# Kernel tuning notes

Measured on AMD Instinct MI355X. Metric: run time of the kernel, lower is better.

The kernel has to match this reference:

```python
import jax, jax.numpy as jnp
import numpy as np

B, L, E, H, FF = 2, 2048, 1024, 16, 4096
DH = E // H
EPS = 1e-5
# NOTE: source has attn_scale = 1 / dh**(-0.5) == sqrt(dh) (multiplies, not divides)
ATTN_SCALE = float(DH) ** 0.5


def _layernorm(x, w, b):
    mu = jnp.mean(x, axis=-1, keepdims=True)
    var = jnp.mean((x - mu) ** 2, axis=-1, keepdims=True)
    return (x - mu) * jax.lax.rsqrt(var + EPS) * w + b


def setup_inputs() -> dict:
    key = jax.random.key(0)
    ks = jax.random.split(key, 8)
    s = 0.02
    return {
        "x": jax.random.normal(ks[0], (B, L, E), jnp.float32),
        "ln1_w": jnp.ones((E,), jnp.float32),
        "ln1_b": jnp.zeros((E,), jnp.float32),
        "wq": jax.random.normal(ks[1], (E, E), jnp.float32) * s,
        "bq": jnp.zeros((E,), jnp.float32),
        "wk": jax.random.normal(ks[2], (E, E), jnp.float32) * s,
        "bk": jnp.zeros((E,), jnp.float32),
        "wv": jax.random.normal(ks[3], (E, E), jnp.float32) * s,
        "bv": jnp.zeros((E,), jnp.float32),
        "wo": jax.random.normal(ks[4], (E, E), jnp.float32) * s,
        "bo": jnp.zeros((E,), jnp.float32),
        "ln2_w": jnp.ones((E,), jnp.float32),
        "ln2_b": jnp.zeros((E,), jnp.float32),
        "wu": jax.random.normal(ks[5], (E, FF), jnp.float32) * s,
        "bu": jnp.zeros((FF,), jnp.float32),
        "wd": jax.random.normal(ks[6], (FF, E), jnp.float32) * s,
        "bd": jnp.zeros((E,), jnp.float32),
    }


def reference(x, ln1_w, ln1_b, wq, bq, wk, bk, wv, bv, wo, bo,
              ln2_w, ln2_b, wu, bu, wd, bd):
    # --- attention block (pre-LN, manual softmax attention) ---
    xn = _layernorm(x, ln1_w, ln1_b)                       # [B,L,E]
    q = (xn @ wq + bq).reshape(B, L, H, DH)
    k = (xn @ wk + bk).reshape(B, L, H, DH)
    v = (xn @ wv + bv).reshape(B, L, H, DH)
    score = jnp.einsum("blhd,bmhd->bhlm", q, k) * ATTN_SCALE  # [B,H,L,L]
    attn = jax.nn.softmax(score, axis=-1)
    ctx = jnp.einsum("bhlm,bmhd->blhd", attn, v).reshape(B, L, E)
    hidden = x + (ctx @ wo + bo)
    # --- FFN block (pre-LN, GELU) ---
    hn = _layernorm(hidden, ln2_w, ln2_b)
    up = jax.nn.gelu(hn @ wu + bu, approximate=False)      # [B,L,F]
    down = up @ wd + bd
    return hidden + down
```

## Files before the change

### kernel.cpp

```cpp
#include <hip/hip_runtime.h>
#include <stdint.h>


typedef __attribute__((ext_vector_type(8))) short short8;
typedef __attribute__((ext_vector_type(4))) float floatx4;
typedef __attribute__((ext_vector_type(16))) float floatx16;

extern "C" __device__ float __ocml_native_exp2_f32(float);
#define EXP2(x) __ocml_native_exp2_f32(x)

#define MFMA_BF16(a, b, c) __builtin_amdgcn_mfma_f32_16x16x32_bf16((a), (b), (c), 0, 0, 0)
#define MFMA32(a, b, c) __builtin_amdgcn_mfma_f32_32x32x16_bf16((a), (b), (c), 0, 0, 0)

__device__ __forceinline__ unsigned short f2bf(float f) {
  union { float f; unsigned int u; } v; v.f = f;
  unsigned int r = v.u + 0x7FFFu + ((v.u >> 16) & 1u);
  return (unsigned short)(r >> 16);
}

__device__ __forceinline__ unsigned int f2u(float f) {
  union { float f; unsigned int u; } v; v.f = f; return v.u;
}

__device__ __forceinline__ short8 pack4(unsigned a, unsigned b, unsigned c, unsigned d) {
  union { unsigned u[4]; short8 s; } v;
  v.u[0] = a; v.u[1] = b; v.u[2] = c; v.u[3] = d;
  return v.s;
}

__device__ __forceinline__ void gl_lds16(const unsigned short* g, unsigned short* l) {
  __builtin_amdgcn_global_load_lds(
      (const __attribute__((address_space(1))) unsigned int*)g,
      (__attribute__((address_space(3))) unsigned int*)l, 16, 0, 0);
}

template <int MODE, int BN>
__global__ __launch_bounds__(256)
void gemm_bt(const unsigned short* __restrict__ A,
             const unsigned short* __restrict__ Bt,
             const float* __restrict__ bias,
             void* __restrict__ outp,
             const float* __restrict__ res,
             int K,
             void* __restrict__ out2, void* __restrict__ out3,
             const float* __restrict__ bias2, const float* __restrict__ bias3) {
  constexpr int BM = 128, BK = 64;
  constexpr int MI = (BN == 128) ? 4 : 2;
  constexpr int NI = 4;
  __shared__ __align__(16) unsigned short As[BM * BK];
  __shared__ __align__(16) unsigned short Bs[BN * BK];
  const int tid = threadIdx.x;
  const int wave = tid >> 6, lane = tid & 63, l16 = lane & 15, quad = lane >> 4;
  const int m0 = blockIdx.y * BM, n0 = blockIdx.x * BN;
  const int wm = (BN == 128) ? (wave >> 1) * 64 : wave * 32;
  const int wn = (BN == 128) ? (wave & 1) * 64 : 0;
  const int sw = l16 & 7;
  const int sl0 = (quad ^ sw) << 3;
  const int sl1 = sl0 ^ 32;

  floatx4 acc[MI][NI] = {};

  for (int k0 = 0; k0 < K; k0 += BK) {
    __syncthreads();
#pragma unroll
    for (int c = 0; c < (BM * BK) / 2048; ++c) {
      const int e = (c * 256 + tid) * 8;
      const int row = e >> 6, c8 = (e >> 3) & 7;
      gl_lds16(A + (size_t)(m0 + row) * K + k0 + ((c8 ^ (row & 7)) << 3), &As[e]);
    }
#pragma unroll
    for (int c = 0; c < (BN * BK) / 2048; ++c) {
      const int e = (c * 256 + tid) * 8;
      const int row = e >> 6, c8 = (e >> 3) & 7;
      gl_lds16(Bt + (size_t)(n0 + row) * K + k0 + ((c8 ^ (row & 7)) << 3), &Bs[e]);
    }
    __syncthreads();

    short8 af0[MI], af1[MI], bf0[NI], bf1[NI];
#pragma unroll
    for (int i = 0; i < MI; ++i) {
      af0[i] = *(const short8*)&As[(wm + i * 16 + l16) * BK + sl0];
      af1[i] = *(const short8*)&As[(wm + i * 16 + l16) * BK + sl1];
    }
#pragma unroll
    for (int i = 0; i < NI; ++i) {
      bf0[i] = *(const short8*)&Bs[(wn + i * 16 + l16) * BK + sl0];
      bf1[i] = *(const short8*)&Bs[(wn + i * 16 + l16) * BK + sl1];
    }
#pragma unroll
    for (int mi = 0; mi < MI; ++mi)
#pragma unroll
      for (int ni = 0; ni < NI; ++ni) {
        acc[mi][ni] = MFMA_BF16(af0[mi], bf0[ni], acc[mi][ni]);
        acc[mi][ni] = MFMA_BF16(af1[mi], bf1[ni], acc[mi][ni]);
      }
  }

  const int seg = (MODE == 0) ? (n0 >> 10) : 0;
  const float* bptr = bias;
  if constexpr (MODE == 0) bptr = (seg == 0) ? bias : (seg == 1 ? bias2 : bias3);

  float bcol[NI];
#pragma unroll
  for (int ni = 0; ni < NI; ++ni) {
    const int n = n0 + wn + ni * 16 + l16;
    bcol[ni] = bptr[(MODE == 0) ? (n & 1023) : n];
  }

#pragma unroll
  for (int mi = 0; mi < MI; ++mi) {
#pragma unroll
    for (int r = 0; r < 4; ++r) {
      const int m = m0 + wm + mi * 16 + quad * 4 + r;
#pragma unroll
      for (int ni = 0; ni < NI; ++ni) {
        const int n = n0 + wn + ni * 16 + l16;
        const float c = acc[mi][ni][r] + bcol[ni];
        if constexpr (MODE == 0) {
          const int b_ = m >> 11, l = m & 2047, hd = n & 1023;
          const size_t idx =
              ((size_t)((b_ * 16 + (hd >> 6)) * 2048 + l)) * 64 + (hd & 63);
          if (seg == 0)       ((unsigned short*)outp)[idx] = f2bf(c * 11.5415603270f);
          else if (seg == 1)  ((unsigned short*)out2)[idx] = f2bf(c);
          else                ((unsigned short*)out3)[idx] = f2bf(c);
        } else if constexpr (MODE == 1) {
          ((float*)outp)[(size_t)m * 1024 + n] = res[(size_t)m * 1024 + n] + c;
        } else if constexpr (MODE == 2) {
          const float g = 0.5f * c * (1.0f + erff(c * 0.70710678118654752f));
          ((unsigned short*)outp)[(size_t)m * 4096 + n] = f2bf(g);
        } else {
          ((float*)outp)[(size_t)m * 1024 + n] = res[(size_t)m * 1024 + n] + c;
        }
      }
    }
  }
}

__global__ __launch_bounds__(256)
void layernorm_kernel(const float* __restrict__ x, const float* __restrict__ w,
                      const float* __restrict__ b, unsigned short* __restrict__ out) {
  const int row = blockIdx.x, tid = threadIdx.x;
  const int wave = tid >> 6, lane = tid & 63;
  const float4 v = ((const float4*)(x + (size_t)row * 1024))[tid];
  float s = v.x + v.y + v.z + v.w;
  float s2 = v.x * v.x + v.y * v.y + v.z * v.z + v.w * v.w;
#pragma unroll
  for (int off = 32; off > 0; off >>= 1) {
    s += __shfl_down(s, off);
    s2 += __shfl_down(s2, off);
  }
  __shared__ float red[8];
  if (lane == 0) { red[wave] = s; red[4 + wave] = s2; }
  __syncthreads();
  const float ts = red[0] + red[1] + red[2] + red[3];
  const float ts2 = red[4] + red[5] + red[6] + red[7];
  const float mu = ts * (1.0f / 1024.0f);
  const float var = ts2 * (1.0f / 1024.0f) - mu * mu;
  const float rs = rsqrtf(var + 1e-5f);
  const float4 wv = ((const float4*)w)[tid];
  const float4 bv = ((const float4*)b)[tid];
  ushort4 o;
  o.x = f2bf((v.x - mu) * rs * wv.x + bv.x);
  o.y = f2bf((v.y - mu) * rs * wv.y + bv.y);
  o.z = f2bf((v.z - mu) * rs * wv.z + bv.z);
  o.w = f2bf((v.w - mu) * rs * wv.w + bv.w);
  ((ushort4*)(out + (size_t)row * 1024))[tid] = o;
}

__global__ __launch_bounds__(256)
void transpose_cast4(const float* __restrict__ s0, const float* __restrict__ s1,
                     const float* __restrict__ s2, const float* __restrict__ s3,
                     unsigned short* __restrict__ dst) {
  __shared__ float tile[32][33];
  const int z = blockIdx.z;
  const float* in = (z == 0) ? s0 : (z == 1) ? s1 : (z == 2) ? s2 : s3;
  unsigned short* out = dst + (size_t)z * 1024 * 1024;
  const int tx = threadIdx.x, ty = threadIdx.y;
  const int c0 = blockIdx.x * 32, r0 = blockIdx.y * 32;
#pragma unroll
  for (int i = 0; i < 4; ++i)
    tile[ty + 8 * i][tx] = in[(size_t)(r0 + ty + 8 * i) * 1024 + c0 + tx];
  __syncthreads();
#pragma unroll
  for (int i = 0; i < 4; ++i)
    out[(size_t)(c0 + ty + 8 * i) * 1024 + r0 + tx] = f2bf(tile[tx][ty + 8 * i]);
}

__global__ __launch_bounds__(256)
void transpose_cast(const float* __restrict__ in, unsigned short* __restrict__ out,
                    int R, int C) {
  __shared__ float tile[32][33];
  const int tx = threadIdx.x, ty = threadIdx.y;
  const int c0 = blockIdx.x * 32, r0 = blockIdx.y * 32;
#pragma unroll
  for (int i = 0; i < 4; ++i)
    tile[ty + 8 * i][tx] = in[(size_t)(r0 + ty + 8 * i) * C + c0 + tx];
  __syncthreads();
#pragma unroll
  for (int i = 0; i < 4; ++i)
    out[(size_t)(c0 + ty + 8 * i) * R + r0 + tx] = f2bf(tile[tx][ty + 8 * i]);
}

__global__ __launch_bounds__(256)
void transpose_bf16(const unsigned short* __restrict__ in,
                    unsigned short* __restrict__ out, int R, int C) {
  __shared__ unsigned short tile[32][33];
  const size_t hoff = (size_t)blockIdx.z * R * C;
  in += hoff; out += hoff;
  const int tx = threadIdx.x, ty = threadIdx.y;
  const int c0 = blockIdx.x * 32, r0 = blockIdx.y * 32;
#pragma unroll
  for (int i = 0; i < 4; ++i)
    tile[ty + 8 * i][tx] = in[(size_t)(r0 + ty + 8 * i) * C + c0 + tx];
  __syncthreads();
  const int txp = (tx & ~12) | ((tx & 4) << 1) | ((tx & 8) >> 1);
#pragma unroll
  for (int i = 0; i < 4; ++i)
    out[(size_t)(c0 + ty + 8 * i) * R + r0 + txp] = tile[tx][ty + 8 * i];
}

__global__ __launch_bounds__(256)
void flash_attn(const unsigned short* __restrict__ q,
                const unsigned short* __restrict__ k,
                const unsigned short* __restrict__ v,
                unsigned short* __restrict__ ctx) {
  __shared__ __align__(16) unsigned short Ks[2][64 * 64];
  __shared__ __align__(16) unsigned short Vs[2][64 * 64];
  const int bh = blockIdx.y, qt = blockIdx.x;
  const int tid = threadIdx.x, wave = tid >> 6, lane = tid & 63;
  const int lo = lane & 31, hi = lane >> 5, sw7 = lo & 7;
  const unsigned short* kb = k + (size_t)bh * 2048 * 64;
  const unsigned short* vb = v + (size_t)bh * 64 * 2048;

  const int qrow = qt * 128 + wave * 32 + lo;
  const unsigned short* qp = q + ((size_t)bh * 2048 + qrow) * 64;
  short8 qf[4];
#pragma unroll
  for (int kq = 0; kq < 4; ++kq) qf[kq] = *(const short8*)(qp + kq * 16 + hi * 8);

  int co[4];
#pragma unroll
  for (int j = 0; j < 4; ++j) co[j] = ((j * 2 + hi) ^ sw7) << 3;

  floatx16 O0 = {}, O1 = {};
  float m_run = -1e30f, l_run = 0.f;

  auto stage = [&](int t, int bufi) {
    const int kv0 = t * 64;
#pragma unroll
    for (int c = 0; c < 2; ++c) {
      const int e = (c * 256 + tid) * 8;
      const int r = e >> 6, ch = (e >> 3) & 7;
      const int sc = ((ch ^ (r & 7)) << 3);
      gl_lds16(kb + (size_t)(kv0 + r) * 64 + sc, &Ks[bufi][e]);
      gl_lds16(vb + (size_t)r * 2048 + kv0 + sc, &Vs[bufi][e]);
    }
  };
  stage(0, 0);

  for (int t = 0; t < 32; ++t) {
    __syncthreads();
    const int bufi = t & 1;
    if (t + 1 < 32) stage(t + 1, bufi ^ 1);

    const unsigned short* Kb = &Ks[bufi][0];
    const unsigned short* Vb = &Vs[bufi][0];

    floatx16 st0 = {}, st1 = {};
#pragma unroll
    for (int kq = 0; kq < 4; ++kq) {
      const short8 kf0 = *(const short8*)&Kb[lo * 64 + co[kq]];
      const short8 kf1 = *(const short8*)&Kb[(32 + lo) * 64 + co[kq]];
      st0 = MFMA32(kf0, qf[kq], st0);
      st1 = MFMA32(kf1, qf[kq], st1);
    }

    float mx = fmaxf(st0[0], st1[0]);
#pragma unroll
    for (int r = 1; r < 16; ++r) mx = fmaxf(mx, fmaxf(st0[r], st1[r]));
    mx = fmaxf(mx, __shfl_xor(mx, 32));
    if (!__all(mx - m_run <= 8.0f)) {
      const float m_new = fmaxf(m_run, mx);
      const float alpha = EXP2(m_run - m_new);
      m_run = m_new;
      l_run *= alpha;
#pragma unroll
      for (int r = 0; r < 16; ++r) { O0[r] *= alpha; O1[r] *= alpha; }
    }
    float rsum = 0.f;
#pragma unroll
    for (int r = 0; r < 16; ++r) {
      st0[r] = EXP2(st0[r] - m_run);
      st1[r] = EXP2(st1[r] - m_run);
      rsum += st0[r] + st1[r];
    }
    rsum += __shfl_xor(rsum, 32);
    l_run += rsum;

    unsigned pw0[8], pw1[8];
#pragma unroll
    for (int i = 0; i < 8; ++i) {
      pw0[i] = __builtin_amdgcn_perm(f2u(st0[2 * i + 1]), f2u(st0[2 * i]), 0x07060302u);
      pw1[i] = __builtin_amdgcn_perm(f2u(st1[2 * i + 1]), f2u(st1[2 * i]), 0x07060302u);
    }
    const short8 pf[4] = { pack4(pw0[0], pw0[1], pw0[2], pw0[3]),
                           pack4(pw0[4], pw0[5], pw0[6], pw0[7]),
                           pack4(pw1[0], pw1[1], pw1[2], pw1[3]),
                           pack4(pw1[4], pw1[5], pw1[6], pw1[7]) };

#pragma unroll
    for (int s = 0; s < 4; ++s) {
      const short8 vf0 = *(const short8*)&Vb[lo * 64 + co[s]];
      const short8 vf1 = *(const short8*)&Vb[(32 + lo) * 64 + co[s]];
      O0 = MFMA32(vf0, pf[s], O0);
      O1 = MFMA32(vf1, pf[s], O1);
    }
  }

  const int b_ = bh >> 4, h_ = bh & 15;
  const float inv = 1.0f / l_run;
  unsigned short* op = ctx + ((size_t)(b_ * 2048) + qrow) * 1024 + h_ * 64;
#pragma unroll
  for (int rq = 0; rq < 4; ++rq) {
    ushort4 a4, b4;
    a4.x = f2bf(O0[rq * 4 + 0] * inv); a4.y = f2bf(O0[rq * 4 + 1] * inv);
    a4.z = f2bf(O0[rq * 4 + 2] * inv); a4.w = f2bf(O0[rq * 4 + 3] * inv);
    *(ushort4*)(op + rq * 8 + hi * 4) = a4;
    b4.x = f2bf(O1[rq * 4 + 0] * inv); b4.y = f2bf(O1[rq * 4 + 1] * inv);
    b4.z = f2bf(O1[rq * 4 + 2] * inv); b4.w = f2bf(O1[rq * 4 + 3] * inv);
    *(ushort4*)(op + 32 + rq * 8 + hi * 4) = b4;
  }
}

extern "C" void kernel_launch(void* const* d_in, const int* in_sizes, int n_in,
                              void* d_out, int out_size, void* d_ws, size_t ws_size,
                              hipStream_t stream) {
  const float* x     = (const float*)d_in[0];
  const float* ln1_w = (const float*)d_in[1];
  const float* ln1_b = (const float*)d_in[2];
  const float* wq    = (const float*)d_in[3];
  const float* bq    = (const float*)d_in[4];
  const float* wk    = (const float*)d_in[5];
  const float* bk    = (const float*)d_in[6];
  const float* wv    = (const float*)d_in[7];
  const float* bv    = (const float*)d_in[8];
  const float* wo    = (const float*)d_in[9];
  const float* bo    = (const float*)d_in[10];
  const float* ln2_w = (const float*)d_in[11];
  const float* ln2_b = (const float*)d_in[12];
  const float* wu    = (const float*)d_in[13];
  const float* bu    = (const float*)d_in[14];
  const float* wd    = (const float*)d_in[15];
  const float* bd    = (const float*)d_in[16];

  char* W = (char*)d_ws;
  const size_t MB = 1ull << 20;
  unsigned short* wqkvT = (unsigned short*)(W + 0 * MB);
  unsigned short* woT   = (unsigned short*)(W + 6 * MB);
  unsigned short* wuT   = (unsigned short*)(W + 8 * MB);
  unsigned short* wdT   = (unsigned short*)(W + 16 * MB);
  unsigned short* xn    = (unsigned short*)(W + 24 * MB);
  unsigned short* qb    = (unsigned short*)(W + 32 * MB);
  unsigned short* kb    = (unsigned short*)(W + 40 * MB);
  unsigned short* vb    = (unsigned short*)(W + 48 * MB);
  unsigned short* cx    = (unsigned short*)(W + 56 * MB);
  float*          hid   = (float*)(W + 64 * MB);
  unsigned short* up    = (unsigned short*)(W + 24 * MB);

  const dim3 tb(32, 8);
  transpose_cast4<<<dim3(32, 32, 4), tb, 0, stream>>>(wq, wk, wv, wo, wqkvT);
  transpose_cast<<<dim3(128, 32), tb, 0, stream>>>(wu, wuT, 1024, 4096);
  transpose_cast<<<dim3(32, 128), tb, 0, stream>>>(wd, wdT, 4096, 1024);

  layernorm_kernel<<<4096, 256, 0, stream>>>(x, ln1_w, ln1_b, xn);
  gemm_bt<0, 128><<<dim3(24, 32), 256, 0, stream>>>(
      xn, wqkvT, bq, qb, nullptr, 1024, kb, cx, bk, bv);
  transpose_bf16<<<dim3(2, 64, 32), tb, 0, stream>>>(cx, vb, 2048, 64);
  flash_attn<<<dim3(16, 32), 256, 0, stream>>>(qb, kb, vb, cx);
  gemm_bt<1, 64><<<dim3(16, 32), 256, 0, stream>>>(
      cx, woT, bo, hid, x, 1024, nullptr, nullptr, nullptr, nullptr);

  layernorm_kernel<<<4096, 256, 0, stream>>>(hid, ln2_w, ln2_b, cx);
  gemm_bt<2, 128><<<dim3(32, 32), 256, 0, stream>>>(
      cx, wuT, bu, up, nullptr, 1024, nullptr, nullptr, nullptr, nullptr);
  gemm_bt<3, 64><<<dim3(16, 32), 256, 0, stream>>>(
      up, wdT, bd, d_out, hid, 4096, nullptr, nullptr, nullptr, nullptr);
}
```

Measured before the change: 378.8 us.

## Double-buffer narrow GEMM tiles and shrink flash-attention blocks to two waves

The BN=64 GEMM variants (output projection and down projection) now double-buffer their LDS tiles, so the next K-tile load overlaps the MFMA work on the current one. Flash attention drops from 4 waves per block to 2 (64 query rows per block, twice as many blocks), which gives more blocks to spread across CUs. It also raises wave priority around the MFMA sections and turns the row max and row sum into tree reductions for more instruction-level parallelism. The cost is extra LDS per GEMM block, and each attention block now reuses its staged K/V tiles across fewer query rows, so K/V loads per query grow.

```diff
diff --git a/kernel.cpp b/kernel.cpp
--- a/kernel.cpp
+++ b/kernel.cpp
@@ -47,8 +47,10 @@
   constexpr int BM = 128, BK = 64;
   constexpr int MI = (BN == 128) ? 4 : 2;
   constexpr int NI = 4;
-  __shared__ __align__(16) unsigned short As[BM * BK];
-  __shared__ __align__(16) unsigned short Bs[BN * BK];
+  constexpr bool DB = (BN == 64);
+  constexpr int NB = DB ? 2 : 1;
+  __shared__ __align__(16) unsigned short As[NB][BM * BK];
+  __shared__ __align__(16) unsigned short Bs[NB][BN * BK];
   const int tid = threadIdx.x;
   const int wave = tid >> 6, lane = tid & 63, l16 = lane & 15, quad = lane >> 4;
   const int m0 = blockIdx.y * BM, n0 = blockIdx.x * BN;
@@ -60,32 +62,32 @@
 
   floatx4 acc[MI][NI] = {};
 
-  for (int k0 = 0; k0 < K; k0 += BK) {
-    __syncthreads();
+  auto stage = [&](int k0, int b) {
 #pragma unroll
     for (int c = 0; c < (BM * BK) / 2048; ++c) {
       const int e = (c * 256 + tid) * 8;
       const int row = e >> 6, c8 = (e >> 3) & 7;
-      gl_lds16(A + (size_t)(m0 + row) * K + k0 + ((c8 ^ (row & 7)) << 3), &As[e]);
+      gl_lds16(A + (size_t)(m0 + row) * K + k0 + ((c8 ^ (row & 7)) << 3), &As[b][e]);
     }
 #pragma unroll
     for (int c = 0; c < (BN * BK) / 2048; ++c) {
       const int e = (c * 256 + tid) * 8;
       const int row = e >> 6, c8 = (e >> 3) & 7;
-      gl_lds16(Bt + (size_t)(n0 + row) * K + k0 + ((c8 ^ (row & 7)) << 3), &Bs[e]);
-    }
-    __syncthreads();
-
+      gl_lds16(Bt + (size_t)(n0 + row) * K + k0 + ((c8 ^ (row & 7)) << 3), &Bs[b][e]);
+    }
+  };
+
+  auto compute = [&](int b) {
     short8 af0[MI], af1[MI], bf0[NI], bf1[NI];
 #pragma unroll
     for (int i = 0; i < MI; ++i) {
-      af0[i] = *(const short8*)&As[(wm + i * 16 + l16) * BK + sl0];
-      af1[i] = *(const short8*)&As[(wm + i * 16 + l16) * BK + sl1];
+      af0[i] = *(const short8*)&As[b][(wm + i * 16 + l16) * BK + sl0];
+      af1[i] = *(const short8*)&As[b][(wm + i * 16 + l16) * BK + sl1];
     }
 #pragma unroll
     for (int i = 0; i < NI; ++i) {
-      bf0[i] = *(const short8*)&Bs[(wn + i * 16 + l16) * BK + sl0];
-      bf1[i] = *(const short8*)&Bs[(wn + i * 16 + l16) * BK + sl1];
+      bf0[i] = *(const short8*)&Bs[b][(wn + i * 16 + l16) * BK + sl0];
+      bf1[i] = *(const short8*)&Bs[b][(wn + i * 16 + l16) * BK + sl1];
     }
 #pragma unroll
     for (int mi = 0; mi < MI; ++mi)
@@ -94,6 +96,25 @@
         acc[mi][ni] = MFMA_BF16(af0[mi], bf0[ni], acc[mi][ni]);
         acc[mi][ni] = MFMA_BF16(af1[mi], bf1[ni], acc[mi][ni]);
       }
+  };
+
+  if constexpr (DB) {
+    stage(0, 0);
+    __syncthreads();
+    const int nt = K / BK;
+    for (int t = 0; t < nt; ++t) {
+      const int b = t & 1;
+      if (t + 1 < nt) stage((t + 1) * BK, b ^ 1);
+      compute(b);
+      __syncthreads();
+    }
+  } else {
+    for (int k0 = 0; k0 < K; k0 += BK) {
+      __syncthreads();
+      stage(k0, 0);
+      __syncthreads();
+      compute(0);
+    }
   }
 
   const int seg = (MODE == 0) ? (n0 >> 10) : 0;
@@ -219,7 +240,7 @@
     out[(size_t)(c0 + ty + 8 * i) * R + r0 + txp] = tile[tx][ty + 8 * i];
 }
 
-__global__ __launch_bounds__(256)
+__global__ __launch_bounds__(128)
 void flash_attn(const unsigned short* __restrict__ q,
                 const unsigned short* __restrict__ k,
                 const unsigned short* __restrict__ v,
@@ -232,7 +253,7 @@
   const unsigned short* kb = k + (size_t)bh * 2048 * 64;
   const unsigned short* vb = v + (size_t)bh * 64 * 2048;
 
-  const int qrow = qt * 128 + wave * 32 + lo;
+  const int qrow = qt * 64 + wave * 32 + lo;
   const unsigned short* qp = q + ((size_t)bh * 2048 + qrow) * 64;
   short8 qf[4];
 #pragma unroll
@@ -248,8 +269,8 @@
   auto stage = [&](int t, int bufi) {
     const int kv0 = t * 64;
 #pragma unroll
-    for (int c = 0; c < 2; ++c) {
-      const int e = (c * 256 + tid) * 8;
+    for (int c = 0; c < 4; ++c) {
+      const int e = (c * 128 + tid) * 8;
       const int r = e >> 6, ch = (e >> 3) & 7;
       const int sc = ((ch ^ (r & 7)) << 3);
       gl_lds16(kb + (size_t)(kv0 + r) * 64 + sc, &Ks[bufi][e]);
@@ -267,6 +288,7 @@
     const unsigned short* Vb = &Vs[bufi][0];
 
     floatx16 st0 = {}, st1 = {};
+    __builtin_amdgcn_s_setprio(1);
 #pragma unroll
     for (int kq = 0; kq < 4; ++kq) {
       const short8 kf0 = *(const short8*)&Kb[lo * 64 + co[kq]];
@@ -274,10 +296,15 @@
       st0 = MFMA32(kf0, qf[kq], st0);
       st1 = MFMA32(kf1, qf[kq], st1);
     }
-
-    float mx = fmaxf(st0[0], st1[0]);
-#pragma unroll
-    for (int r = 1; r < 16; ++r) mx = fmaxf(mx, fmaxf(st0[r], st1[r]));
+    __builtin_amdgcn_s_setprio(0);
+
+    float mp[8];
+#pragma unroll
+    for (int r = 0; r < 8; ++r)
+      mp[r] = fmaxf(fmaxf(st0[r], st0[r + 8]), fmaxf(st1[r], st1[r + 8]));
+    mp[0] = fmaxf(fmaxf(mp[0], mp[1]), fmaxf(mp[2], mp[3]));
+    mp[4] = fmaxf(fmaxf(mp[4], mp[5]), fmaxf(mp[6], mp[7]));
+    float mx = fmaxf(mp[0], mp[4]);
     mx = fmaxf(mx, __shfl_xor(mx, 32));
     if (!__all(mx - m_run <= 8.0f)) {
       const float m_new = fmaxf(m_run, mx);
@@ -287,13 +314,18 @@
 #pragma unroll
       for (int r = 0; r < 16; ++r) { O0[r] *= alpha; O1[r] *= alpha; }
     }
-    float rsum = 0.f;
 #pragma unroll
     for (int r = 0; r < 16; ++r) {
       st0[r] = EXP2(st0[r] - m_run);
       st1[r] = EXP2(st1[r] - m_run);
-      rsum += st0[r] + st1[r];
-    }
+    }
+    float sp[8];
+#pragma unroll
+    for (int r = 0; r < 8; ++r)
+      sp[r] = (st0[r] + st0[r + 8]) + (st1[r] + st1[r + 8]);
+    sp[0] = (sp[0] + sp[1]) + (sp[2] + sp[3]);
+    sp[4] = (sp[4] + sp[5]) + (sp[6] + sp[7]);
+    float rsum = sp[0] + sp[4];
     rsum += __shfl_xor(rsum, 32);
     l_run += rsum;
 
@@ -308,6 +340,7 @@
                            pack4(pw1[0], pw1[1], pw1[2], pw1[3]),
                            pack4(pw1[4], pw1[5], pw1[6], pw1[7]) };
 
+    __builtin_amdgcn_s_setprio(1);
 #pragma unroll
     for (int s = 0; s < 4; ++s) {
       const short8 vf0 = *(const short8*)&Vb[lo * 64 + co[s]];
@@ -315,6 +348,7 @@
       O0 = MFMA32(vf0, pf[s], O0);
       O1 = MFMA32(vf1, pf[s], O1);
     }
+    __builtin_amdgcn_s_setprio(0);
   }
 
   const int b_ = bh >> 4, h_ = bh & 15;
@@ -376,7 +410,7 @@
   gemm_bt<0, 128><<<dim3(24, 32), 256, 0, stream>>>(
       xn, wqkvT, bq, qb, nullptr, 1024, kb, cx, bk, bv);
   transpose_bf16<<<dim3(2, 64, 32), tb, 0, stream>>>(cx, vb, 2048, 64);
-  flash_attn<<<dim3(16, 32), 256, 0, stream>>>(qb, kb, vb, cx);
+  flash_attn<<<dim3(32, 32), 128, 0, stream>>>(qb, kb, vb, cx);
   gemm_bt<1, 64><<<dim3(16, 32), 256, 0, stream>>>(
       cx, woT, bo, hid, x, 1024, nullptr, nullptr, nullptr, nullptr);
 
```

Measured after the change: 380.2 us. No clear change (+0.4%).

## Split attention KV tile across wave pairs and merge partial softmax in LDS

Applied to the files above, without the earlier changes.

The flash attention block now covers 64 query rows instead of 128. Each pair of waves splits every 64-key tile into two 32-key halves, and the two online-softmax partial results are merged at the end through shared memory. The grid doubles to 1024 blocks, which gives more parallelism and occupancy on the many CUs and halves the per-wave score work. It also adds setprio around the MFMA phases and an occupancy hint in launch_bounds. In exchange, K and V tiles are loaded twice as often per query, and there is extra LDS traffic and a barrier for the merge.

```diff
diff --git a/kernel.cpp b/kernel.cpp
--- a/kernel.cpp
+++ b/kernel.cpp
@@ -219,7 +219,7 @@
     out[(size_t)(c0 + ty + 8 * i) * R + r0 + txp] = tile[tx][ty + 8 * i];
 }
 
-__global__ __launch_bounds__(256)
+__global__ __launch_bounds__(256, 4)
 void flash_attn(const unsigned short* __restrict__ q,
                 const unsigned short* __restrict__ k,
                 const unsigned short* __restrict__ v,
@@ -228,11 +228,12 @@
   __shared__ __align__(16) unsigned short Vs[2][64 * 64];
   const int bh = blockIdx.y, qt = blockIdx.x;
   const int tid = threadIdx.x, wave = tid >> 6, lane = tid & 63;
+  const int qw = wave & 1, kw = wave >> 1;
   const int lo = lane & 31, hi = lane >> 5, sw7 = lo & 7;
   const unsigned short* kb = k + (size_t)bh * 2048 * 64;
   const unsigned short* vb = v + (size_t)bh * 64 * 2048;
 
-  const int qrow = qt * 128 + wave * 32 + lo;
+  const int qrow = qt * 64 + qw * 32 + lo;
   const unsigned short* qp = q + ((size_t)bh * 2048 + qrow) * 64;
   short8 qf[4];
 #pragma unroll
@@ -266,18 +267,20 @@
     const unsigned short* Kb = &Ks[bufi][0];
     const unsigned short* Vb = &Vs[bufi][0];
 
-    floatx16 st0 = {}, st1 = {};
+    floatx16 st = {};
+    __builtin_amdgcn_s_setprio(1);
 #pragma unroll
     for (int kq = 0; kq < 4; ++kq) {
-      const short8 kf0 = *(const short8*)&Kb[lo * 64 + co[kq]];
-      const short8 kf1 = *(const short8*)&Kb[(32 + lo) * 64 + co[kq]];
-      st0 = MFMA32(kf0, qf[kq], st0);
-      st1 = MFMA32(kf1, qf[kq], st1);
-    }
-
-    float mx = fmaxf(st0[0], st1[0]);
-#pragma unroll
-    for (int r = 1; r < 16; ++r) mx = fmaxf(mx, fmaxf(st0[r], st1[r]));
+      const short8 kf = *(const short8*)&Kb[(kw * 32 + lo) * 64 + co[kq]];
+      st = MFMA32(kf, qf[kq], st);
+    }
+    __builtin_amdgcn_s_setprio(0);
+
+    float mp[4];
+#pragma unroll
+    for (int r = 0; r < 4; ++r)
+      mp[r] = fmaxf(fmaxf(st[r], st[r + 4]), fmaxf(st[r + 8], st[r + 12]));
+    float mx = fmaxf(fmaxf(mp[0], mp[1]), fmaxf(mp[2], mp[3]));
     mx = fmaxf(mx, __shfl_xor(mx, 32));
     if (!__all(mx - m_run <= 8.0f)) {
       const float m_new = fmaxf(m_run, mx);
@@ -287,48 +290,76 @@
 #pragma unroll
       for (int r = 0; r < 16; ++r) { O0[r] *= alpha; O1[r] *= alpha; }
     }
-    float rsum = 0.f;
-#pragma unroll
-    for (int r = 0; r < 16; ++r) {
-      st0[r] = EXP2(st0[r] - m_run);
-      st1[r] = EXP2(st1[r] - m_run);
-      rsum += st0[r] + st1[r];
-    }
+#pragma unroll
+    for (int r = 0; r < 16; ++r) st[r] = EXP2(st[r] - m_run);
+    float sp[4];
+#pragma unroll
+    for (int r = 0; r < 4; ++r)
+      sp[r] = (st[r] + st[r + 4]) + (st[r + 8] + st[r + 12]);
+    float rsum = (sp[0] + sp[1]) + (sp[2] + sp[3]);
     rsum += __shfl_xor(rsum, 32);
     l_run += rsum;
 
-    unsigned pw0[8], pw1[8];
-#pragma unroll
-    for (int i = 0; i < 8; ++i) {
-      pw0[i] = __builtin_amdgcn_perm(f2u(st0[2 * i + 1]), f2u(st0[2 * i]), 0x07060302u);
-      pw1[i] = __builtin_amdgcn_perm(f2u(st1[2 * i + 1]), f2u(st1[2 * i]), 0x07060302u);
-    }
-    const short8 pf[4] = { pack4(pw0[0], pw0[1], pw0[2], pw0[3]),
-                           pack4(pw0[4], pw0[5], pw0[6], pw0[7]),
-                           pack4(pw1[0], pw1[1], pw1[2], pw1[3]),
-                           pack4(pw1[4], pw1[5], pw1[6], pw1[7]) };
-
-#pragma unroll
-    for (int s = 0; s < 4; ++s) {
-      const short8 vf0 = *(const short8*)&Vb[lo * 64 + co[s]];
-      const short8 vf1 = *(const short8*)&Vb[(32 + lo) * 64 + co[s]];
-      O0 = MFMA32(vf0, pf[s], O0);
-      O1 = MFMA32(vf1, pf[s], O1);
-    }
-  }
-
-  const int b_ = bh >> 4, h_ = bh & 15;
-  const float inv = 1.0f / l_run;
-  unsigned short* op = ctx + ((size_t)(b_ * 2048) + qrow) * 1024 + h_ * 64;
-#pragma unroll
-  for (int rq = 0; rq < 4; ++rq) {
-    ushort4 a4, b4;
-    a4.x = f2bf(O0[rq * 4 + 0] * inv); a4.y = f2bf(O0[rq * 4 + 1] * inv);
-    a4.z = f2bf(O0[rq * 4 + 2] * inv); a4.w = f2bf(O0[rq * 4 + 3] * inv);
-    *(ushort4*)(op + rq * 8 + hi * 4) = a4;
-    b4.x = f2bf(O1[rq * 4 + 0] * inv); b4.y = f2bf(O1[rq * 4 + 1] * inv);
-    b4.z = f2bf(O1[rq * 4 + 2] * inv); b4.w = f2bf(O1[rq * 4 + 3] * inv);
-    *(ushort4*)(op + 32 + rq * 8 + hi * 4) = b4;
+    unsigned pw[8];
+#pragma unroll
+    for (int i = 0; i < 8; ++i)
+      pw[i] = __builtin_amdgcn_perm(f2u(st[2 * i + 1]), f2u(st[2 * i]), 0x07060302u);
+    const short8 pf0 = pack4(pw[0], pw[1], pw[2], pw[3]);
+    const short8 pf1 = pack4(pw[4], pw[5], pw[6], pw[7]);
+
+    __builtin_amdgcn_s_setprio(1);
+    {
+      const short8 vf00 = *(const short8*)&Vb[lo * 64 + co[2 * kw]];
+      const short8 vf01 = *(const short8*)&Vb[(32 + lo) * 64 + co[2 * kw]];
+      O0 = MFMA32(vf00, pf0, O0);
+      O1 = MFMA32(vf01, pf0, O1);
+      const short8 vf10 = *(const short8*)&Vb[lo * 64 + co[2 * kw + 1]];
+      const short8 vf11 = *(const short8*)&Vb[(32 + lo) * 64 + co[2 * kw + 1]];
+      O0 = MFMA32(vf10, pf1, O0);
+      O1 = MFMA32(vf11, pf1, O1);
+    }
+    __builtin_amdgcn_s_setprio(0);
+  }
+
+  __syncthreads();
+  float* Os = (float*)&Ks[0][0];
+  float* Ml = (float*)&Vs[0][0];
+  if (kw == 1) {
+    float* o = Os + (size_t)(qw * 64 + lane) * 32;
+#pragma unroll
+    for (int r = 0; r < 16; ++r) {
+      o[(r + lane) & 31] = O0[r];
+      o[(16 + r + lane) & 31] = O1[r];
+    }
+    Ml[qw * 64 + lane] = m_run;
+    Ml[128 + qw * 64 + lane] = l_run;
+  }
+  __syncthreads();
+  if (kw == 0) {
+    const float m2 = Ml[qw * 64 + lane];
+    const float l2 = Ml[128 + qw * 64 + lane];
+    const float m = fmaxf(m_run, m2);
+    const float a1 = EXP2(m_run - m), a2 = EXP2(m2 - m);
+    const float linv = 1.0f / (l_run * a1 + l2 * a2);
+    const float* o = Os + (size_t)(qw * 64 + lane) * 32;
+    float f0[16], f1[16];
+#pragma unroll
+    for (int r = 0; r < 16; ++r) {
+      f0[r] = (O0[r] * a1 + o[(r + lane) & 31] * a2) * linv;
+      f1[r] = (O1[r] * a1 + o[(16 + r + lane) & 31] * a2) * linv;
+    }
+    const int b_ = bh >> 4, h_ = bh & 15;
+    unsigned short* op = ctx + ((size_t)(b_ * 2048) + qrow) * 1024 + h_ * 64;
+#pragma unroll
+    for (int rq = 0; rq < 4; ++rq) {
+      ushort4 a4, b4;
+      a4.x = f2bf(f0[rq * 4 + 0]); a4.y = f2bf(f0[rq * 4 + 1]);
+      a4.z = f2bf(f0[rq * 4 + 2]); a4.w = f2bf(f0[rq * 4 + 3]);
+      *(ushort4*)(op + rq * 8 + hi * 4) = a4;
+      b4.x = f2bf(f1[rq * 4 + 0]); b4.y = f2bf(f1[rq * 4 + 1]);
+      b4.z = f2bf(f1[rq * 4 + 2]); b4.w = f2bf(f1[rq * 4 + 3]);
+      *(ushort4*)(op + 32 + rq * 8 + hi * 4) = b4;
+    }
   }
 }
 
@@ -376,7 +407,7 @@
   gemm_bt<0, 128><<<dim3(24, 32), 256, 0, stream>>>(
       xn, wqkvT, bq, qb, nullptr, 1024, kb, cx, bk, bv);
   transpose_bf16<<<dim3(2, 64, 32), tb, 0, stream>>>(cx, vb, 2048, 64);
-  flash_attn<<<dim3(16, 32), 256, 0, stream>>>(qb, kb, vb, cx);
+  flash_attn<<<dim3(32, 32), 256, 0, stream>>>(qb, kb, vb, cx);
   gemm_bt<1, 64><<<dim3(16, 32), 256, 0, stream>>>(
       cx, woT, bo, hid, x, 1024, nullptr, nullptr, nullptr, nullptr);
 
```

After: 403.6 us. 6.6% more time.
